# Performance work log

Measured on AMD Instinct MI355X. Metric: run time of the kernel, lower is better.

## Reference

```python
import jax, jax.numpy as jnp
import numpy as np

B, T = 64, 1024
ATTN_DIM, RNN_DIM, ENC_DIM = 128, 1024, 512
N_FILT, KSIZE = 32, 31
PAD = (KSIZE - 1) // 2


def setup_inputs() -> dict:
    key = jax.random.key(0)
    ks = jax.random.split(key, 11)
    query = jax.random.normal(ks[0], (B, RNN_DIM), dtype=jnp.float32)
    keys = jax.random.normal(ks[1], (B, T, ENC_DIM), dtype=jnp.float32)
    values = jax.random.normal(ks[2], (B, T, ENC_DIM), dtype=jnp.float32)
    attention_weights_cum = jax.random.uniform(ks[3], (B, T), dtype=jnp.float32)
    mask = jnp.zeros((B, T), dtype=bool)
    s = 0.02
    W_loc_conv = jax.random.normal(ks[4], (N_FILT, 1, KSIZE), dtype=jnp.float32) * s
    W_loc_proj = jax.random.normal(ks[5], (ATTN_DIM, N_FILT), dtype=jnp.float32) * s
    W_query = jax.random.normal(ks[6], (ATTN_DIM, RNN_DIM), dtype=jnp.float32) * s
    W_key = jax.random.normal(ks[7], (ATTN_DIM, ENC_DIM), dtype=jnp.float32) * s
    W_value = jax.random.normal(ks[8], (ENC_DIM, ENC_DIM), dtype=jnp.float32) * s
    W_attn = jax.random.normal(ks[9], (1, ATTN_DIM), dtype=jnp.float32) * s
    return {
        "query": query, "keys": keys, "values": values,
        "attention_weights_cum": attention_weights_cum, "mask": mask,
        "W_loc_conv": W_loc_conv, "W_loc_proj": W_loc_proj,
        "W_query": W_query, "W_key": W_key, "W_value": W_value, "W_attn": W_attn,
    }


def reference(query, keys, values, attention_weights_cum, mask,
              W_loc_conv, W_loc_proj, W_query, W_key, W_value, W_attn):
    # location features: conv1d over cumulative attention, (B,1,T) -> (B,N_FILT,T)
    loc = jax.lax.conv_general_dilated(
        attention_weights_cum[:, None, :], W_loc_conv,
        window_strides=(1,), padding=[(PAD, PAD)],
        dimension_numbers=("NCH", "OIH", "NCH"))
    # (B,T,N_FILT) @ W_loc_proj.T -> (B,T,ATTN_DIM)
    loc_feat = jnp.einsum("bft,af->bta", loc, W_loc_proj)
    q_proj = query @ W_query.T                      # (B, ATTN_DIM)
    k_proj = jnp.einsum("bte,ae->bta", keys, W_key)  # (B, T, ATTN_DIM)
    energies = jnp.tanh(q_proj[:, None, :] + k_proj + loc_feat)
    scores = jnp.einsum("bta,a->bt", energies, W_attn[0])  # (B, T)
    scores = jnp.where(mask, -jnp.inf, scores)
    attn = jax.nn.softmax(scores, axis=-1)
    v_proj = jnp.einsum("bte,fe->btf", values, W_value)  # (B, T, ENC_DIM)
    context = jnp.einsum("bt,btf->bf", attn, v_proj)      # (B, ENC_DIM)
    return context, attn
```

## Files before the change

kernel.cpp:

```cpp
#include <hip/hip_runtime.h>
#include <math.h>

#define B_   64
#define T_   1024
#define AD   128
#define RD   1024
#define ED   512
#define NF   32
#define KS   31
#define PADW 15

typedef short bf16x8 __attribute__((ext_vector_type(8)));
typedef float f32x4  __attribute__((ext_vector_type(4)));

typedef __attribute__((address_space(1))) unsigned gu32;
typedef __attribute__((address_space(3))) unsigned lu32;

__device__ __forceinline__ void gll16(const void* g, void* l) {
  __builtin_amdgcn_global_load_lds(
      (gu32*)(unsigned long long)g,
      (lu32*)(unsigned)(unsigned long long)l, 16, 0, 0);
}

__device__ __forceinline__ short f2bf(float x) {
  union { float f; unsigned u; } v; v.f = x;
  unsigned r = (v.u + 0x7FFFu + ((v.u >> 16) & 1u)) >> 16;
  return (short)r;
}

__device__ __forceinline__ float tanh_fast(float x) {
  float t = __expf(2.0f * x);
  return (t - 1.0f) * __builtin_amdgcn_rcpf(t + 1.0f);
}

#define KB_  2048
__global__ __launch_bounds__(256) void prep_kernel(
    const float* __restrict__ keys, const float* __restrict__ Wk,
    const float* __restrict__ Wlp, const float* __restrict__ awc,
    const float* __restrict__ Wc, const float* __restrict__ query,
    const float* __restrict__ Wq, short* __restrict__ keys16,
    short* __restrict__ Wk16, short* __restrict__ Wlp16,
    short* __restrict__ loc_g, float* __restrict__ qp) {
  __shared__ float sh_awc[128 + KS - 1];
  __shared__ float sh_wc[NF * KS];
  __shared__ float sh_q[RD];
  __shared__ float sh_red[AD];
  const int blk = blockIdx.x, tid = threadIdx.x;

  if (blk < KB_) {
    size_t base = (size_t)blk * 4096 + tid;
#pragma unroll
    for (int i = 0; i < 16; ++i) {
      size_t p = base + (size_t)i * 256;
      float4 v = *(const float4*)&keys[p * 4];
      short4 h = { f2bf(v.x), f2bf(v.y), f2bf(v.z), f2bf(v.w) };
      *(short4*)&keys16[p * 4] = h;
    }
  } else if (blk < KB_ + 68) {
    int p = (blk - KB_) * 256 + tid;
    const float* src; short* dst; int off;
    if (p < 16384) { src = Wk; dst = Wk16; off = p; }
    else           { src = Wlp; dst = Wlp16; off = p - 16384; }
    float4 v = *(const float4*)&src[off * 4];
    short4 h = { f2bf(v.x), f2bf(v.y), f2bf(v.z), f2bf(v.w) };
    *(short4*)&dst[off * 4] = h;
  } else if (blk < KB_ + 68 + 512) {
    int cb = blk - (KB_ + 68);
    int b = cb >> 3, t0 = (cb & 7) * 128;
    for (int i = tid; i < NF * KS; i += 256) sh_wc[i] = Wc[i];
    if (tid < 128 + KS - 1) {
      int gt = t0 - PADW + tid;
      sh_awc[tid] = (gt >= 0 && gt < T_) ? awc[b * T_ + gt] : 0.0f;
    }
    __syncthreads();
    const int t = tid & 127, fh = (tid >> 7) * 16;
    for (int fq = 0; fq < 4; ++fq) {
      float s0 = 0.f, s1 = 0.f, s2 = 0.f, s3 = 0.f;
      const float* w0 = &sh_wc[(fh + fq * 4 + 0) * KS];
      const float* w1 = &sh_wc[(fh + fq * 4 + 1) * KS];
      const float* w2 = &sh_wc[(fh + fq * 4 + 2) * KS];
      const float* w3 = &sh_wc[(fh + fq * 4 + 3) * KS];
#pragma unroll
      for (int k = 0; k < KS; ++k) {
        float aw = sh_awc[t + k];
        s0 += w0[k] * aw; s1 += w1[k] * aw; s2 += w2[k] * aw; s3 += w3[k] * aw;
      }
      short4 h = { f2bf(s0), f2bf(s1), f2bf(s2), f2bf(s3) };
      *(short4*)&loc_g[((size_t)(b * T_ + t0 + t)) * NF + fh + fq * 4] = h;
    }
  } else {
    int b = blk - (KB_ + 68 + 512);
    *(float4*)&sh_q[tid * 4] = *(const float4*)&query[b * RD + tid * 4];
    __syncthreads();
    const int a = tid & 127, kh = tid >> 7;
    const float* wr = &Wq[(size_t)a * RD + kh * 512];
    const float* qr = &sh_q[kh * 512];
    float acc = 0.f;
    for (int e = 0; e < 512; e += 4) {
      float4 w = *(const float4*)&wr[e];
      acc += w.x * qr[e] + w.y * qr[e + 1] + w.z * qr[e + 2] + w.w * qr[e + 3];
    }
    if (kh == 1) sh_red[a] = acc;
    __syncthreads();
    if (kh == 0) qp[b * AD + a] = acc + sh_red[a];
  }
}

__global__ __launch_bounds__(256, 2) void scores_kernel(
    const short* __restrict__ keys16, const short* __restrict__ Wk16,
    const short* __restrict__ Wlp16, const short* __restrict__ loc_g,
    const float* __restrict__ qp, const float* __restrict__ Wa,
    float* __restrict__ scores) {
  __shared__ alignas(16) short As[128 * 64];
  __shared__ alignas(16) short Bs[128 * 64];
  __shared__ float qp_s[AD], wa_s[AD];
  __shared__ float sc_s[128 * 2];

  const int tid = threadIdx.x;
  const int b = blockIdx.y, t0 = blockIdx.x * 128;
  const int lane = tid & 63, wave = tid >> 6;
  const int wm = wave >> 1, wn = wave & 1;
  const int m16 = lane & 15, s4 = lane >> 4;

  if (tid < AD) { qp_s[tid] = qp[b * AD + tid]; wa_s[tid] = Wa[tid]; }

  {
    const int r = lane >> 2, cb = lane & 3;
#pragma unroll
    for (int i = 0; i < 2; ++i) {
      int row = wave * 32 + i * 16;
      gll16(&loc_g[((size_t)(b * T_ + t0 + row + r)) * NF + cb * 8],
            &As[row * 32]);
      gll16(&Wlp16[(row + r) * NF + cb * 8], &Bs[row * 32]);
    }
  }
  __syncthreads();

  f32x4 acc[4][4];
  {
    bf16x8 af[4], bfr[4];
#pragma unroll
    for (int mt = 0; mt < 4; ++mt)
      af[mt] = *(const bf16x8*)&As[(wm * 64 + mt * 16 + m16) * 32 + s4 * 8];
#pragma unroll
    for (int nt = 0; nt < 4; ++nt)
      bfr[nt] = *(const bf16x8*)&Bs[(wn * 64 + nt * 16 + m16) * 32 + s4 * 8];
#pragma unroll
    for (int mt = 0; mt < 4; ++mt)
#pragma unroll
      for (int nt = 0; nt < 4; ++nt)
        acc[mt][nt] = __builtin_amdgcn_mfma_f32_16x16x32_bf16(
            af[mt], bfr[nt], (f32x4){0.f, 0.f, 0.f, 0.f}, 0, 0, 0);
  }

  const int r8 = lane >> 3, cb8 = lane & 7;
  const int cbg = cb8 ^ r8;
  const size_t kb = ((size_t)(b * T_ + t0)) * ED;

  for (int kc = 0; kc < 8; ++kc) {
    __syncthreads();
#pragma unroll
    for (int i = 0; i < 4; ++i) {
      int row = wave * 32 + i * 8;
      gll16(&keys16[kb + (size_t)(row + r8) * ED + kc * 64 + cbg * 8],
            &As[row * 64]);
      gll16(&Wk16[(size_t)(row + r8) * ED + kc * 64 + cbg * 8],
            &Bs[row * 64]);
    }
    __syncthreads();
#pragma unroll
    for (int kk2 = 0; kk2 < 2; ++kk2) {
      const int j = kk2 * 4 + s4;
      const int ca = (j ^ (m16 & 7)) * 8;
      bf16x8 af[4], bfr[4];
#pragma unroll
      for (int mt = 0; mt < 4; ++mt)
        af[mt] = *(const bf16x8*)&As[(wm * 64 + mt * 16 + m16) * 64 + ca];
#pragma unroll
      for (int nt = 0; nt < 4; ++nt)
        bfr[nt] = *(const bf16x8*)&Bs[(wn * 64 + nt * 16 + m16) * 64 + ca];
#pragma unroll
      for (int mt = 0; mt < 4; ++mt)
#pragma unroll
        for (int nt = 0; nt < 4; ++nt)
          acc[mt][nt] = __builtin_amdgcn_mfma_f32_16x16x32_bf16(
              af[mt], bfr[nt], acc[mt][nt], 0, 0, 0);
    }
  }

  float qv[4], wv[4];
#pragma unroll
  for (int nt = 0; nt < 4; ++nt) {
    int a = wn * 64 + nt * 16 + m16;
    qv[nt] = qp_s[a]; wv[nt] = wa_s[a];
  }
#pragma unroll
  for (int mt = 0; mt < 4; ++mt) {
#pragma unroll
    for (int r = 0; r < 4; ++r) {
      float p = 0.f;
#pragma unroll
      for (int nt = 0; nt < 4; ++nt)
        p += wv[nt] * tanh_fast(acc[mt][nt][r] + qv[nt]);
      p += __shfl_xor(p, 1); p += __shfl_xor(p, 2);
      p += __shfl_xor(p, 4); p += __shfl_xor(p, 8);
      if (m16 == 0) sc_s[(wm * 64 + mt * 16 + s4 * 4 + r) * 2 + wn] = p;
    }
  }
  __syncthreads();
  if (tid < 128)
    scores[(size_t)b * T_ + t0 + tid] = sc_s[tid * 2] + sc_s[tid * 2 + 1];
}

__global__ __launch_bounds__(256) void softmax_kernel(
    const float* __restrict__ scores, const unsigned char* __restrict__ mask,
    float* __restrict__ attn) {
  const int b = blockIdx.x, tid = threadIdx.x;
  __shared__ float redm[4], reds[4];

  float4 s4 = *(const float4*)&scores[b * T_ + tid * 4];
  uchar4 m4 = *(const uchar4*)&mask[b * T_ + tid * 4];
  if (m4.x) s4.x = -INFINITY;
  if (m4.y) s4.y = -INFINITY;
  if (m4.z) s4.z = -INFINITY;
  if (m4.w) s4.w = -INFINITY;

  float mx = fmaxf(fmaxf(s4.x, s4.y), fmaxf(s4.z, s4.w));
#pragma unroll
  for (int off = 32; off >= 1; off >>= 1) mx = fmaxf(mx, __shfl_xor(mx, off, 64));
  if ((tid & 63) == 0) redm[tid >> 6] = mx;
  __syncthreads();
  mx = fmaxf(fmaxf(redm[0], redm[1]), fmaxf(redm[2], redm[3]));

  float e0 = expf(s4.x - mx), e1 = expf(s4.y - mx);
  float e2 = expf(s4.z - mx), e3 = expf(s4.w - mx);
  float sum = e0 + e1 + e2 + e3;
#pragma unroll
  for (int off = 32; off >= 1; off >>= 1) sum += __shfl_xor(sum, off, 64);
  if ((tid & 63) == 0) reds[tid >> 6] = sum;
  __syncthreads();
  sum = reds[0] + reds[1] + reds[2] + reds[3];

  float inv = 1.0f / sum;
  float4 o4 = { e0 * inv, e1 * inv, e2 * inv, e3 * inv };
  *(float4*)&attn[b * T_ + tid * 4] = o4;
}

__global__ __launch_bounds__(256) void wvsum_kernel(
    const float* __restrict__ values, const float* __restrict__ attn,
    float* __restrict__ wvp) {
  const int tc = blockIdx.x, b = blockIdx.y, tid = threadIdx.x;
  __shared__ float at_s[64];
  if (tid < 64) at_s[tid] = attn[b * T_ + tc * 64 + tid];
  __syncthreads();
  const int e4 = tid & 127, th = tid >> 7;
  const float* vb =
      values + ((size_t)(b * T_ + tc * 64 + th * 32)) * ED + e4 * 4;
  float4 acc = {0.f, 0.f, 0.f, 0.f};
#pragma unroll 8
  for (int t = 0; t < 32; ++t) {
    float a = at_s[th * 32 + t];
    float4 v = *(const float4*)&vb[(size_t)t * ED];
    acc.x = fmaf(a, v.x, acc.x); acc.y = fmaf(a, v.y, acc.y);
    acc.z = fmaf(a, v.z, acc.z); acc.w = fmaf(a, v.w, acc.w);
  }
  *(float4*)&wvp[((size_t)(b * 32 + tc * 2 + th)) * ED + e4 * 4] = acc;
}

__global__ __launch_bounds__(256) void context_kernel(
    const float* __restrict__ wvp, const float* __restrict__ Wv,
    float* __restrict__ ctx) {
  const int fq = blockIdx.x, b = blockIdx.y, tid = threadIdx.x;
  __shared__ float wv_s[ED];
  __shared__ float red[128];
  for (int e = tid; e < ED; e += 256) {
    float s = 0.f;
    const float* base = &wvp[(size_t)b * 32 * ED + e];
#pragma unroll
    for (int p = 0; p < 32; ++p) s += base[p * ED];
    wv_s[e] = s;
  }
  __syncthreads();
  const int fl = tid & 127, eh = tid >> 7;
  const int f = fq * 128 + fl;
  const float* wr = &Wv[(size_t)f * ED + eh * 256];
  const float* qr = &wv_s[eh * 256];
  float acc = 0.f;
  for (int e = 0; e < 256; e += 4) {
    float4 w = *(const float4*)&wr[e];
    acc += w.x * qr[e] + w.y * qr[e + 1] + w.z * qr[e + 2] + w.w * qr[e + 3];
  }
  if (eh == 1) red[fl] = acc;
  __syncthreads();
  if (eh == 0) ctx[b * ED + f] = acc + red[fl];
}

extern "C" void kernel_launch(void* const* d_in, const int* in_sizes, int n_in,
                              void* d_out, int out_size, void* d_ws, size_t ws_size,
                              hipStream_t stream) {
  const float* query = (const float*)d_in[0];
  const float* keys  = (const float*)d_in[1];
  const float* values= (const float*)d_in[2];
  const float* awc   = (const float*)d_in[3];
  const unsigned char* mask = (const unsigned char*)d_in[4];
  const float* Wc    = (const float*)d_in[5];
  const float* Wlp   = (const float*)d_in[6];
  const float* Wq    = (const float*)d_in[7];
  const float* Wk    = (const float*)d_in[8];
  const float* Wv    = (const float*)d_in[9];
  const float* Wa    = (const float*)d_in[10];

  float* ctx  = (float*)d_out;
  float* attn = (float*)d_out + B_ * ED;

  float* ws = (float*)d_ws;
  float* qp      = ws;
  float* scoresB = qp + B_ * AD;
  float* wvp     = scoresB + B_ * T_;
  short* Wk16    = (short*)(wvp + (size_t)B_ * 32 * ED);
  short* Wlp16   = Wk16 + AD * ED;
  short* loc_g   = Wlp16 + AD * NF;
  short* keys16  = loc_g + (size_t)B_ * T_ * NF;

  prep_kernel<<<KB_ + 68 + 512 + 64, 256, 0, stream>>>(
      keys, Wk, Wlp, awc, Wc, query, Wq, keys16, Wk16, Wlp16, loc_g, qp);
  scores_kernel<<<dim3(8, B_), 256, 0, stream>>>(keys16, Wk16, Wlp16, loc_g,
                                                 qp, Wa, scoresB);
  softmax_kernel<<<B_, 256, 0, stream>>>(scoresB, mask, attn);
  wvsum_kernel<<<dim3(16, B_), 256, 0, stream>>>(values, attn, wvp);
  context_kernel<<<dim3(4, B_), 256, 0, stream>>>(wvp, Wv, ctx);
}
```

Before: 349.4 us.

## Fuse keys bf16 conversion into scores kernel with register prefetch; split wvsum finer

Drops the separate pass that converted all keys to bf16 in the prep kernel. The scores kernel now loads fp32 keys directly into registers, prefetching the next K-chunk while the current one computes, converts them to bf16 and writes them into swizzled LDS. This removes a full fp32 read plus bf16 write and re-read of the 128MB keys tensor. Separately, wvsum is split into twice as many blocks, each loading 8 rows at once for more memory parallelism, and context_kernel now reduces 64 partials instead of 32. The cost is more register pressure and extra syncs in the scores loop.

```diff
diff --git a/kernel.cpp b/kernel.cpp
--- a/kernel.cpp
+++ b/kernel.cpp
@@ -33,12 +33,10 @@
   return (t - 1.0f) * __builtin_amdgcn_rcpf(t + 1.0f);
 }
 
-#define KB_  2048
 __global__ __launch_bounds__(256) void prep_kernel(
-    const float* __restrict__ keys, const float* __restrict__ Wk,
-    const float* __restrict__ Wlp, const float* __restrict__ awc,
-    const float* __restrict__ Wc, const float* __restrict__ query,
-    const float* __restrict__ Wq, short* __restrict__ keys16,
+    const float* __restrict__ Wk, const float* __restrict__ Wlp,
+    const float* __restrict__ awc, const float* __restrict__ Wc,
+    const float* __restrict__ query, const float* __restrict__ Wq,
     short* __restrict__ Wk16, short* __restrict__ Wlp16,
     short* __restrict__ loc_g, float* __restrict__ qp) {
   __shared__ float sh_awc[128 + KS - 1];
@@ -47,25 +45,16 @@
   __shared__ float sh_red[AD];
   const int blk = blockIdx.x, tid = threadIdx.x;
 
-  if (blk < KB_) {
-    size_t base = (size_t)blk * 4096 + tid;
-#pragma unroll
-    for (int i = 0; i < 16; ++i) {
-      size_t p = base + (size_t)i * 256;
-      float4 v = *(const float4*)&keys[p * 4];
-      short4 h = { f2bf(v.x), f2bf(v.y), f2bf(v.z), f2bf(v.w) };
-      *(short4*)&keys16[p * 4] = h;
-    }
-  } else if (blk < KB_ + 68) {
-    int p = (blk - KB_) * 256 + tid;
+  if (blk < 68) {
+    int p = blk * 256 + tid;
     const float* src; short* dst; int off;
     if (p < 16384) { src = Wk; dst = Wk16; off = p; }
     else           { src = Wlp; dst = Wlp16; off = p - 16384; }
     float4 v = *(const float4*)&src[off * 4];
     short4 h = { f2bf(v.x), f2bf(v.y), f2bf(v.z), f2bf(v.w) };
     *(short4*)&dst[off * 4] = h;
-  } else if (blk < KB_ + 68 + 512) {
-    int cb = blk - (KB_ + 68);
+  } else if (blk < 68 + 512) {
+    int cb = blk - 68;
     int b = cb >> 3, t0 = (cb & 7) * 128;
     for (int i = tid; i < NF * KS; i += 256) sh_wc[i] = Wc[i];
     if (tid < 128 + KS - 1) {
@@ -89,7 +78,7 @@
       *(short4*)&loc_g[((size_t)(b * T_ + t0 + t)) * NF + fh + fq * 4] = h;
     }
   } else {
-    int b = blk - (KB_ + 68 + 512);
+    int b = blk - (68 + 512);
     *(float4*)&sh_q[tid * 4] = *(const float4*)&query[b * RD + tid * 4];
     __syncthreads();
     const int a = tid & 127, kh = tid >> 7;
@@ -107,7 +96,7 @@
 }
 
 __global__ __launch_bounds__(256, 2) void scores_kernel(
-    const short* __restrict__ keys16, const short* __restrict__ Wk16,
+    const float* __restrict__ keys, const short* __restrict__ Wk16,
     const short* __restrict__ Wlp16, const short* __restrict__ loc_g,
     const float* __restrict__ qp, const float* __restrict__ Wa,
     float* __restrict__ scores) {
@@ -122,6 +111,33 @@
   const int wm = wave >> 1, wn = wave & 1;
   const int m16 = lane & 15, s4 = lane >> 4;
 
+  const int sr = tid >> 3;
+  const int sg = tid & 7;
+  const int swz = (sg ^ (sr & 7)) * 8;
+  const float* kA = &keys[((size_t)(b * T_ + t0 + sr)) * ED + sg * 8];
+
+  float4 bufA[8], bufB[8];
+  auto LOADA = [&](float4 (&buf)[8], int kc) {
+#pragma unroll
+    for (int i = 0; i < 4; ++i) {
+      const float* p = kA + (size_t)i * 32 * ED + (size_t)kc * 64;
+      buf[2 * i]     = *(const float4*)p;
+      buf[2 * i + 1] = *(const float4*)(p + 4);
+    }
+  };
+  auto WRITEA = [&](float4 (&buf)[8]) {
+#pragma unroll
+    for (int i = 0; i < 4; ++i) {
+      bf16x8 h = { f2bf(buf[2*i].x),   f2bf(buf[2*i].y),
+                   f2bf(buf[2*i].z),   f2bf(buf[2*i].w),
+                   f2bf(buf[2*i+1].x), f2bf(buf[2*i+1].y),
+                   f2bf(buf[2*i+1].z), f2bf(buf[2*i+1].w) };
+      *(bf16x8*)&As[(sr + i * 32) * 64 + swz] = h;
+    }
+  };
+
+  LOADA(bufA, 0);
+
   if (tid < AD) { qp_s[tid] = qp[b * AD + tid]; wa_s[tid] = Wa[tid]; }
 
   {
@@ -155,19 +171,16 @@
 
   const int r8 = lane >> 3, cb8 = lane & 7;
   const int cbg = cb8 ^ r8;
-  const size_t kb = ((size_t)(b * T_ + t0)) * ED;
-
-  for (int kc = 0; kc < 8; ++kc) {
-    __syncthreads();
+
+  auto STAGEB = [&](int kc) {
 #pragma unroll
     for (int i = 0; i < 4; ++i) {
       int row = wave * 32 + i * 8;
-      gll16(&keys16[kb + (size_t)(row + r8) * ED + kc * 64 + cbg * 8],
-            &As[row * 64]);
-      gll16(&Wk16[(size_t)(row + r8) * ED + kc * 64 + cbg * 8],
+      gll16(&Wk16[(size_t)(row + r8) * ED + (size_t)kc * 64 + cbg * 8],
             &Bs[row * 64]);
     }
-    __syncthreads();
+  };
+  auto COMPUTE = [&]() {
 #pragma unroll
     for (int kk2 = 0; kk2 < 2; ++kk2) {
       const int j = kk2 * 4 + s4;
@@ -186,6 +199,21 @@
           acc[mt][nt] = __builtin_amdgcn_mfma_f32_16x16x32_bf16(
               af[mt], bfr[nt], acc[mt][nt], 0, 0, 0);
     }
+  };
+
+  for (int kc = 0; kc < 8; kc += 2) {
+    __syncthreads();
+    WRITEA(bufA);
+    STAGEB(kc);
+    __syncthreads();
+    LOADA(bufB, kc + 1);
+    COMPUTE();
+    __syncthreads();
+    WRITEA(bufB);
+    STAGEB(kc + 1);
+    __syncthreads();
+    if (kc < 6) LOADA(bufA, kc + 2);
+    COMPUTE();
   }
 
   float qv[4], wv[4];
@@ -250,21 +278,28 @@
     const float* __restrict__ values, const float* __restrict__ attn,
     float* __restrict__ wvp) {
   const int tc = blockIdx.x, b = blockIdx.y, tid = threadIdx.x;
-  __shared__ float at_s[64];
-  if (tid < 64) at_s[tid] = attn[b * T_ + tc * 64 + tid];
+  __shared__ float at_s[32];
+  if (tid < 32) at_s[tid] = attn[b * T_ + tc * 32 + tid];
   __syncthreads();
   const int e4 = tid & 127, th = tid >> 7;
   const float* vb =
-      values + ((size_t)(b * T_ + tc * 64 + th * 32)) * ED + e4 * 4;
+      values + ((size_t)(b * T_ + tc * 32 + th * 16)) * ED + e4 * 4;
+  const float* as = &at_s[th * 16];
   float4 acc = {0.f, 0.f, 0.f, 0.f};
-#pragma unroll 8
-  for (int t = 0; t < 32; ++t) {
-    float a = at_s[th * 32 + t];
-    float4 v = *(const float4*)&vb[(size_t)t * ED];
-    acc.x = fmaf(a, v.x, acc.x); acc.y = fmaf(a, v.y, acc.y);
-    acc.z = fmaf(a, v.z, acc.z); acc.w = fmaf(a, v.w, acc.w);
-  }
-  *(float4*)&wvp[((size_t)(b * 32 + tc * 2 + th)) * ED + e4 * 4] = acc;
+#pragma unroll
+  for (int t8 = 0; t8 < 16; t8 += 8) {
+    float4 v[8];
+#pragma unroll
+    for (int u = 0; u < 8; ++u)
+      v[u] = *(const float4*)&vb[(size_t)(t8 + u) * ED];
+#pragma unroll
+    for (int u = 0; u < 8; ++u) {
+      float a = as[t8 + u];
+      acc.x = fmaf(a, v[u].x, acc.x); acc.y = fmaf(a, v[u].y, acc.y);
+      acc.z = fmaf(a, v[u].z, acc.z); acc.w = fmaf(a, v[u].w, acc.w);
+    }
+  }
+  *(float4*)&wvp[((size_t)(b * 64 + tc * 2 + th)) * ED + e4 * 4] = acc;
 }
 
 __global__ __launch_bounds__(256) void context_kernel(
@@ -275,9 +310,9 @@
   __shared__ float red[128];
   for (int e = tid; e < ED; e += 256) {
     float s = 0.f;
-    const float* base = &wvp[(size_t)b * 32 * ED + e];
-#pragma unroll
-    for (int p = 0; p < 32; ++p) s += base[p * ED];
+    const float* base = &wvp[(size_t)b * 64 * ED + e];
+#pragma unroll 16
+    for (int p = 0; p < 64; ++p) s += base[p * ED];
     wv_s[e] = s;
   }
   __syncthreads();
@@ -317,16 +352,15 @@
   float* qp      = ws;
   float* scoresB = qp + B_ * AD;
   float* wvp     = scoresB + B_ * T_;
-  short* Wk16    = (short*)(wvp + (size_t)B_ * 32 * ED);
+  short* Wk16    = (short*)(wvp + (size_t)B_ * 64 * ED);
   short* Wlp16   = Wk16 + AD * ED;
   short* loc_g   = Wlp16 + AD * NF;
-  short* keys16  = loc_g + (size_t)B_ * T_ * NF;
-
-  prep_kernel<<<KB_ + 68 + 512 + 64, 256, 0, stream>>>(
-      keys, Wk, Wlp, awc, Wc, query, Wq, keys16, Wk16, Wlp16, loc_g, qp);
-  scores_kernel<<<dim3(8, B_), 256, 0, stream>>>(keys16, Wk16, Wlp16, loc_g,
+
+  prep_kernel<<<68 + 512 + 64, 256, 0, stream>>>(Wk, Wlp, awc, Wc, query, Wq,
+                                                 Wk16, Wlp16, loc_g, qp);
+  scores_kernel<<<dim3(8, B_), 256, 0, stream>>>(keys, Wk16, Wlp16, loc_g,
                                                  qp, Wa, scoresB);
   softmax_kernel<<<B_, 256, 0, stream>>>(scoresB, mask, attn);
-  wvsum_kernel<<<dim3(16, B_), 256, 0, stream>>>(values, attn, wvp);
+  wvsum_kernel<<<dim3(32, B_), 256, 0, stream>>>(values, attn, wvp);
   context_kernel<<<dim3(4, B_), 256, 0, stream>>>(wvp, Wv, ctx);
 }
```

Result: faster. 340.4 us (-2.6%).
